# Optimization experiments

Measured on AMD Instinct MI355X. Metric: run time of the kernel, lower is better.

The kernel has to match this reference:

```python
import jax, jax.numpy as jnp
import numpy as np

D_MODEL = 1024
N_HEADS = 16
HEAD_DIM = D_MODEL // N_HEADS
SCALE = HEAD_DIM ** -0.5
NEG = -9e15


def setup_inputs() -> dict:
    key = jax.random.key(0)
    k1, k2, k3 = jax.random.split(key, 3)
    B, S = 4, 2048
    x = jax.random.normal(k1, (B, S, D_MODEL), dtype=jnp.float32)
    W_qkv = jax.random.normal(k2, (D_MODEL, 3 * D_MODEL), dtype=jnp.float32) * (D_MODEL ** -0.5)
    b_qkv = jnp.zeros((3 * D_MODEL,), dtype=jnp.float32)
    W_out = jax.random.normal(k3, (D_MODEL, D_MODEL), dtype=jnp.float32) * (D_MODEL ** -0.5)
    b_out = jnp.zeros((D_MODEL,), dtype=jnp.float32)
    return {"x": x, "W_qkv": W_qkv, "b_qkv": b_qkv, "W_out": W_out, "b_out": b_out}


def reference(x, W_qkv, b_qkv, W_out, b_out):
    B, S, _ = x.shape
    qkv = x @ W_qkv + b_qkv                      # [B,S,3D]
    q, k, v = jnp.split(qkv, 3, axis=-1)
    def heads(t):
        return t.reshape(B, S, N_HEADS, HEAD_DIM).transpose(0, 2, 1, 3)  # [B,H,S,d]
    q, k, v = heads(q), heads(k), heads(v)
    logits = jnp.einsum('bhqd,bhkd->bhqk', q, k) * SCALE
    causal = jnp.tril(jnp.ones((S, S), dtype=bool))
    logits = jnp.where(causal[None, None], logits, jnp.float32(NEG))
    attn = jax.nn.softmax(logits, axis=-1)       # dropout p=0 -> identity
    vals = jnp.einsum('bhqk,bhkd->bhqd', attn, v)
    vals = vals.transpose(0, 2, 1, 3).reshape(B, S, D_MODEL)
    return vals @ W_out + b_out
```

## Files before the change

kernel.cpp:

```cpp
#include <hip/hip_runtime.h>

typedef unsigned short u16;
typedef unsigned int u32;
typedef __attribute__((ext_vector_type(8))) short bf16x8;
typedef __attribute__((ext_vector_type(4))) float f32x4;

#define MFMA16(a, b, c) __builtin_amdgcn_mfma_f32_16x16x32_bf16((a), (b), (c), 0, 0, 0)

constexpr int D = 1024;
constexpr int NH = 16;
constexpr int HD = 64;
constexpr int BB = 4;
constexpr int SS = 2048;
constexpr int BH = BB * NH;
constexpr int MTOK = BB * SS;
constexpr float SCALE_LOG2E = 0.125f * 1.44269504088896340736f;

__device__ __forceinline__ u16 f32_bf16(float f) {
  union { float f; u32 u; } v; v.f = f;
  u32 u = v.u;
  u += 0x7FFFu + ((u >> 16) & 1u);
  return (u16)(u >> 16);
}

__device__ __forceinline__ float exp2_fast(float x) {
  float r; asm("v_exp_f32 %0, %1" : "=v"(r) : "v"(x)); return r;
}
__device__ __forceinline__ u16 cvt_bf16_1(float f) {
  u32 r; asm("v_cvt_pk_bf16_f32 %0, %1, %1" : "=v"(r) : "v"(f)); return (u16)r;
}

__device__ __forceinline__ void gload_lds16(const void* g, u16* l) {
  __builtin_amdgcn_global_load_lds(
      (const __attribute__((address_space(1))) u32*)g,
      (__attribute__((address_space(3))) u32*)l, 16, 0, 0);
}

__global__ __launch_bounds__(256)
void cvt_bf16(const float* __restrict__ in, u16* __restrict__ out, int n4) {
  int i = blockIdx.x * 256 + threadIdx.x;
  const int stride = gridDim.x * 256;
  for (; i < n4; i += stride) {
    float4 v = reinterpret_cast<const float4*>(in)[i];
    u32 lo = (u32)f32_bf16(v.x) | ((u32)f32_bf16(v.y) << 16);
    u32 hi = (u32)f32_bf16(v.z) | ((u32)f32_bf16(v.w) << 16);
    reinterpret_cast<uint2*>(out)[i] = make_uint2(lo, hi);
  }
}

__global__ __launch_bounds__(256)
void transpose_bf16(const float* __restrict__ in, u16* __restrict__ out, int R, int C) {
  __shared__ float tile[32][33];
  const int c0 = blockIdx.x * 32, r0 = blockIdx.y * 32;
  const int tx = threadIdx.x, ty = threadIdx.y;
#pragma unroll
  for (int i = 0; i < 4; i++)
    tile[ty + 8 * i][tx] = in[(size_t)(r0 + ty + 8 * i) * C + c0 + tx];
  __syncthreads();
#pragma unroll
  for (int i = 0; i < 4; i++)
    out[(size_t)(c0 + ty + 8 * i) * R + r0 + tx] = f32_bf16(tile[tx][ty + 8 * i]);
}

template <int MODE>
__global__ __launch_bounds__(256)
void gemm_bf16(const u16* __restrict__ A, const u16* __restrict__ Bt,
               const float* __restrict__ bias,
               u16* __restrict__ q_out, u16* __restrict__ k_out,
               u16* __restrict__ vt_out, float* __restrict__ f_out,
               int M, int N, int K) {
  constexpr int BK = 32;
  __shared__ u16 lds_a[3][128 * BK];
  __shared__ u16 lds_b[3][128 * BK];
  const int m0 = blockIdx.x * 128;
  const int n0 = blockIdx.y * 128;
  const int t = threadIdx.x;
  const int lane = t & 63;
  const int w = t >> 6;
  const int wr = w >> 1, wc = w & 1;
  const int fr = lane & 15, fq = lane >> 4;

  const int srow = t >> 2;
  const int schunk = (t & 3) ^ ((srow >> 1) & 3);
  const u16* ga0 = A + (size_t)(m0 + srow) * K + schunk * 8;
  const u16* ga1 = ga0 + (size_t)64 * K;
  const u16* gb0 = Bt + (size_t)(n0 + srow) * K + schunk * 8;
  const u16* gb1 = gb0 + (size_t)64 * K;

  const int swz = ((fr >> 1) & 3) << 4;

#define GSTAGE(bufi, koff)                                                    \
  {                                                                           \
    gload_lds16(ga0 + (koff), lds_a[bufi] + t * 8);                           \
    gload_lds16(ga1 + (koff), lds_a[bufi] + (t + 256) * 8);                   \
    gload_lds16(gb0 + (koff), lds_b[bufi] + t * 8);                           \
    gload_lds16(gb1 + (koff), lds_b[bufi] + (t + 256) * 8);                   \
  }

  f32x4 acc[4][4] = {};
  const int nt = K / BK;

  GSTAGE(0, 0);
  GSTAGE(1, BK);

  int cur = 0;
  for (int kt = 0; kt < nt; ++kt) {
    if (kt + 1 < nt)
      asm volatile("s_waitcnt vmcnt(4)" ::: "memory");
    else
      asm volatile("s_waitcnt vmcnt(0)" ::: "memory");
    __builtin_amdgcn_s_barrier();
    __builtin_amdgcn_sched_barrier(0);

    const char* ca = (const char*)lds_a[cur];
    const char* cb = (const char*)lds_b[cur];
    bf16x8 af[4], bfr[4];
#pragma unroll
    for (int i = 0; i < 4; i++)
      af[i] = *reinterpret_cast<const bf16x8*>(
          ca + (wr * 64 + i * 16 + fr) * 64 + ((fq * 16) ^ swz));
#pragma unroll
    for (int i = 0; i < 4; i++)
      bfr[i] = *reinterpret_cast<const bf16x8*>(
          cb + (wc * 64 + i * 16 + fr) * 64 + ((fq * 16) ^ swz));
    __builtin_amdgcn_s_setprio(1);
#pragma unroll
    for (int i = 0; i < 4; i++)
#pragma unroll
      for (int j = 0; j < 4; j++)
        acc[i][j] = MFMA16(af[i], bfr[j], acc[i][j]);
    __builtin_amdgcn_s_setprio(0);

    if (kt + 2 < nt) {
      const int bufn = cur >= 1 ? cur - 1 : 2;
      GSTAGE(bufn, (kt + 2) * BK);
    }
    cur = cur == 2 ? 0 : cur + 1;
  }
#undef GSTAGE

#pragma unroll
  for (int i = 0; i < 4; i++) {
#pragma unroll
    for (int j = 0; j < 4; j++) {
      const int ncol = n0 + wc * 64 + j * 16 + fr;
      const float bs = bias[ncol];
#pragma unroll
      for (int r = 0; r < 4; r++) {
        const int mrow = m0 + wr * 64 + i * 16 + fq * 4 + r;
        const float vv = acc[i][j][r] + bs;
        if (MODE == 0) {
          const int which = ncol >> 10;
          const int rem = ncol & 1023;
          const int hh = rem >> 6, dd = rem & 63;
          const int bb = mrow >> 11, ss = mrow & 2047;
          const int bh = bb * 16 + hh;
          if (which == 0)
            q_out[((size_t)bh * SS + ss) * HD + dd] = f32_bf16(vv * SCALE_LOG2E);
          else if (which == 1)
            k_out[((size_t)bh * SS + ss) * HD + dd] = f32_bf16(vv);
          else
            vt_out[((size_t)bh * HD + dd) * SS + ss] = f32_bf16(vv);
        } else {
          f_out[(size_t)mrow * N + ncol] = vv;
        }
      }
    }
  }
}

__global__ __launch_bounds__(512)
void attn_fwd(const u16* __restrict__ Qb, const u16* __restrict__ Kb,
              const u16* __restrict__ Vt, u16* __restrict__ vals) {
  const int bid = blockIdx.x;
  const int wk = (bid & 7) * 64 + (bid >> 3);
  const int bh = wk >> 3;
  const int pA = wk & 7;
  const int qtA = pA, qtB = 15 - pA;
  const int nA = 2 * qtA + 2;
  const int nTot = 34;
  const u16* Qp = Qb + (size_t)bh * SS * HD;
  const char* Kp = (const char*)(Kb + (size_t)bh * SS * HD);
  const char* Vp = (const char*)(Vt + (size_t)bh * HD * SS);
  const int t = threadIdx.x, lane = t & 63, w = t >> 6;
  const int fr = lane & 15, fq = lane >> 4;
  const int swz = (fr & 7) << 4;

  __shared__ u16 kbuf[3][4096];
  __shared__ u16 vbuf[3][4096];
  __shared__ u16 plds[8][16][72];
  u16* myp = &plds[w][0][0];

  const int lin = t * 16;

  int offKV[8];
#pragma unroll
  for (int kf = 0; kf < 4; kf++)
#pragma unroll
    for (int kk = 0; kk < 2; kk++)
      offKV[kf * 2 + kk] = (kf * 16 + fr) * 128 + ((kk * 64 + fq * 16) ^ swz);

  bf16x8 aq[2];
  {
    const int qbase = qtA * 128 + w * 16;
#pragma unroll
    for (int kk = 0; kk < 2; kk++)
      aq[kk] = *reinterpret_cast<const bf16x8*>(Qp + (size_t)(qbase + fr) * HD + kk * 32 + fq * 8);
  }

  f32x4 o[4] = {};
  float mrun[4], lpart[4];
#pragma unroll
  for (int j = 0; j < 4; j++) { mrun[j] = -3e38f; lpart[j] = 0.f; }

#define STAGE(bufi, kvt_)                                                     \
  {                                                                           \
    const int row = lin >> 7, colb = lin & 127;                               \
    const int scol = colb ^ ((row & 7) << 4);                                 \
    gload_lds16(Kp + (size_t)((kvt_) * 64 + row) * 128 + scol,                \
                &kbuf[bufi][lin >> 1]);                                       \
    gload_lds16(Vp + (size_t)row * 4096 + (kvt_) * 128 + scol,                \
                &vbuf[bufi][lin >> 1]);                                       \
  }
#define KVIDX(ti_) ((ti_) >= nA ? (ti_) - nA : (ti_))

  auto write_out = [&](int qt) {
    const int b_ = bh >> 4, h_ = bh & 15;
    const int qb = qt * 128 + w * 16;
    float linv[4];
#pragma unroll
    for (int j = 0; j < 4; j++) {
      float rs = lpart[j];
#pragma unroll
      for (int off = 1; off < 16; off <<= 1)
        rs += __shfl_xor(rs, off, 64);
      linv[j] = 1.f / rs;
    }
#pragma unroll
    for (int df = 0; df < 4; df++)
#pragma unroll
      for (int j = 0; j < 4; j++) {
        const float vv = o[df][j] * linv[j];
        const int qg = qb + fq * 4 + j;
        vals[((size_t)(b_ * SS + qg)) * D + h_ * HD + df * 16 + fr] = cvt_bf16_1(vv);
      }
  };

  int cur = 0;
  STAGE(0, 0);
  STAGE(1, 1);

  for (int ti = 0; ti < nTot; ++ti) {
    const bool segB = ti >= nA;
    const int kvt = segB ? ti - nA : ti;
    const int qt = segB ? qtB : qtA;

    if (ti + 1 < nTot)
      asm volatile("s_waitcnt vmcnt(2)" ::: "memory");
    else
      asm volatile("s_waitcnt vmcnt(0)" ::: "memory");
    __builtin_amdgcn_s_barrier();
    __builtin_amdgcn_sched_barrier(0);

    if (ti == nA) {
      write_out(qtA);
      const int qbase = qtB * 128 + w * 16;
#pragma unroll
      for (int kk = 0; kk < 2; kk++)
        aq[kk] = *reinterpret_cast<const bf16x8*>(Qp + (size_t)(qbase + fr) * HD + kk * 32 + fq * 8);
#pragma unroll
      for (int j = 0; j < 4; j++) { mrun[j] = -3e38f; lpart[j] = 0.f; }
#pragma unroll
      for (int df = 0; df < 4; df++) o[df] = f32x4{0.f, 0.f, 0.f, 0.f};
    }

    const char* kb = (const char*)kbuf[cur];
    const char* vb = (const char*)vbuf[cur];

    f32x4 sc[4] = {};
    __builtin_amdgcn_s_setprio(1);
#pragma unroll
    for (int kf = 0; kf < 4; kf++) {
#pragma unroll
      for (int kk = 0; kk < 2; kk++) {
        bf16x8 bk = *reinterpret_cast<const bf16x8*>(kb + offKV[kf * 2 + kk]);
        sc[kf] = MFMA16(aq[kk], bk, sc[kf]);
      }
    }
    __builtin_amdgcn_s_setprio(0);
    if ((kvt >> 1) == qt) {
      const int kg0 = kvt * 64 + fr;
      const int rg0 = qt * 128 + w * 16 + fq * 4;
#pragma unroll
      for (int kf = 0; kf < 4; kf++)
#pragma unroll
        for (int j = 0; j < 4; j++)
          if (kg0 + kf * 16 > rg0 + j) sc[kf][j] = -3e38f;
    }
    float mj[4];
#pragma unroll
    for (int j = 0; j < 4; j++) {
      float m = fmaxf(fmaxf(sc[0][j], sc[1][j]), fmaxf(sc[2][j], sc[3][j]));
#pragma unroll
      for (int off = 1; off < 16; off <<= 1)
        m = fmaxf(m, __shfl_xor(m, off, 64));
      mj[j] = m;
    }
    const bool need = (mj[0] > mrun[0] + 8.f) | (mj[1] > mrun[1] + 8.f) |
                      (mj[2] > mrun[2] + 8.f) | (mj[3] > mrun[3] + 8.f);
    if (__any((int)need)) {
#pragma unroll
      for (int j = 0; j < 4; j++) {
        const float mnew = fmaxf(mrun[j], mj[j]);
        const float alpha = exp2_fast(mrun[j] - mnew);
        mrun[j] = mnew;
        lpart[j] *= alpha;
#pragma unroll
        for (int df = 0; df < 4; df++) o[df][j] *= alpha;
      }
    }
#pragma unroll
    for (int j = 0; j < 4; j++) {
#pragma unroll
      for (int kf = 0; kf < 4; kf++) {
        const float p = exp2_fast(sc[kf][j] - mrun[j]);
        sc[kf][j] = p;
        lpart[j] += p;
      }
    }
#pragma unroll
    for (int kf = 0; kf < 4; kf++)
#pragma unroll
      for (int j = 0; j < 4; j++)
        myp[(fq * 4 + j) * 72 + kf * 16 + fr] = cvt_bf16_1(sc[kf][j]);
    bf16x8 pa[2];
#pragma unroll
    for (int kk = 0; kk < 2; kk++)
      pa[kk] = *reinterpret_cast<const bf16x8*>(myp + fr * 72 + kk * 32 + fq * 8);
    __builtin_amdgcn_s_setprio(1);
#pragma unroll
    for (int df = 0; df < 4; df++) {
#pragma unroll
      for (int kk = 0; kk < 2; kk++) {
        bf16x8 bv = *reinterpret_cast<const bf16x8*>(vb + offKV[df * 2 + kk]);
        o[df] = MFMA16(pa[kk], bv, o[df]);
      }
    }
    __builtin_amdgcn_s_setprio(0);

    const int nxt = ti + 2;
    if (nxt < nTot) {
      const int bufn = cur >= 1 ? cur - 1 : 2;
      STAGE(bufn, KVIDX(nxt));
    }
    cur = cur == 2 ? 0 : cur + 1;
  }
  write_out(qtB);
#undef STAGE
#undef KVIDX
}

extern "C" void kernel_launch(void* const* d_in, const int* in_sizes, int n_in,
                              void* d_out, int out_size, void* d_ws, size_t ws_size,
                              hipStream_t stream) {
  const float* x = (const float*)d_in[0];
  const float* Wqkv = (const float*)d_in[1];
  const float* bqkv = (const float*)d_in[2];
  const float* Wout = (const float*)d_in[3];
  const float* bout = (const float*)d_in[4];
  float* out = (float*)d_out;

  char* p = (char*)d_ws;
  u16* xb = (u16*)p;    p += (size_t)MTOK * D * 2;
  u16* wqkvT = (u16*)p; p += (size_t)3 * D * D * 2;
  u16* woutT = (u16*)p; p += (size_t)D * D * 2;
  u16* Qb = (u16*)p;    p += (size_t)BH * SS * HD * 2;
  u16* Kb = (u16*)p;    p += (size_t)BH * SS * HD * 2;
  u16* Vt = (u16*)p;    p += (size_t)BH * SS * HD * 2;
  u16* vals = (u16*)p;  p += (size_t)MTOK * D * 2;

  cvt_bf16<<<2048, 256, 0, stream>>>(x, xb, MTOK * D / 4);
  transpose_bf16<<<dim3(3 * D / 32, D / 32), dim3(32, 8), 0, stream>>>(Wqkv, wqkvT, D, 3 * D);
  transpose_bf16<<<dim3(D / 32, D / 32), dim3(32, 8), 0, stream>>>(Wout, woutT, D, D);
  gemm_bf16<0><<<dim3(MTOK / 128, 3 * D / 128), 256, 0, stream>>>(
      xb, wqkvT, bqkv, Qb, Kb, Vt, nullptr, MTOK, 3 * D, D);
  attn_fwd<<<dim3(512), 512, 0, stream>>>(Qb, Kb, Vt, vals);
  gemm_bf16<1><<<dim3(MTOK / 128, D / 128), 256, 0, stream>>>(
      vals, woutT, bout, nullptr, nullptr, nullptr, out, MTOK, D, D);
}
```

Baseline: 192.1 us.

## Transpose QK^T MFMA so each lane owns one query row in softmax

Swaps the MFMA operand order for the score computation so the accumulator layout gives each lane a single query row across key columns. The row max and row sum then need only two cross-lane shuffles instead of four per row, per-row state shrinks to scalars, and P is written to LDS as packed bf16 pairs. Rescale factors and the final normalizer are broadcast back to the O layout with shuffles, which adds some shuffle work when rescaling and at output time.

```diff
diff --git a/kernel.cpp b/kernel.cpp
--- a/kernel.cpp
+++ b/kernel.cpp
@@ -28,6 +28,9 @@
 }
 __device__ __forceinline__ u16 cvt_bf16_1(float f) {
   u32 r; asm("v_cvt_pk_bf16_f32 %0, %1, %1" : "=v"(r) : "v"(f)); return (u16)r;
+}
+__device__ __forceinline__ u32 cvt_pk2(float lo, float hi) {
+  u32 r; asm("v_cvt_pk_bf16_f32 %0, %1, %2" : "=v"(r) : "v"(lo), "v"(hi)); return r;
 }
 
 __device__ __forceinline__ void gload_lds16(const void* g, u16* l) {
@@ -209,9 +212,7 @@
   }
 
   f32x4 o[4] = {};
-  float mrun[4], lpart[4];
-#pragma unroll
-  for (int j = 0; j < 4; j++) { mrun[j] = -3e38f; lpart[j] = 0.f; }
+  float mrun = -3e38f, lpart = 0.f;
 
 #define STAGE(bufi, kvt_)                                                     \
   {                                                                           \
@@ -227,20 +228,19 @@
   auto write_out = [&](int qt) {
     const int b_ = bh >> 4, h_ = bh & 15;
     const int qb = qt * 128 + w * 16;
-    float linv[4];
-#pragma unroll
-    for (int j = 0; j < 4; j++) {
-      float rs = lpart[j];
-#pragma unroll
-      for (int off = 1; off < 16; off <<= 1)
-        rs += __shfl_xor(rs, off, 64);
-      linv[j] = 1.f / rs;
-    }
+    float rs = lpart;
+    rs += __shfl_xor(rs, 16, 64);
+    rs += __shfl_xor(rs, 32, 64);
+    const float linv = 1.f / rs;
+    float lj[4];
+#pragma unroll
+    for (int j = 0; j < 4; j++)
+      lj[j] = __shfl(linv, (lane & 48) + fq * 4 + j, 64);
 #pragma unroll
     for (int df = 0; df < 4; df++)
 #pragma unroll
       for (int j = 0; j < 4; j++) {
-        const float vv = o[df][j] * linv[j];
+        const float vv = o[df][j] * lj[j];
         const int qg = qb + fq * 4 + j;
         vals[((size_t)(b_ * SS + qg)) * D + h_ * HD + df * 16 + fr] = cvt_bf16_1(vv);
       }
@@ -268,8 +268,7 @@
 #pragma unroll
       for (int kk = 0; kk < 2; kk++)
         aq[kk] = *reinterpret_cast<const bf16x8*>(Qp + (size_t)(qbase + fr) * HD + kk * 32 + fq * 8);
-#pragma unroll
-      for (int j = 0; j < 4; j++) { mrun[j] = -3e38f; lpart[j] = 0.f; }
+      mrun = -3e38f; lpart = 0.f;
 #pragma unroll
       for (int df = 0; df < 4; df++) o[df] = f32x4{0.f, 0.f, 0.f, 0.f};
     }
@@ -284,55 +283,57 @@
 #pragma unroll
       for (int kk = 0; kk < 2; kk++) {
         bf16x8 bk = *reinterpret_cast<const bf16x8*>(kb + offKV[kf * 2 + kk]);
-        sc[kf] = MFMA16(aq[kk], bk, sc[kf]);
+        sc[kf] = MFMA16(bk, aq[kk], sc[kf]);
       }
     }
     __builtin_amdgcn_s_setprio(0);
     if ((kvt >> 1) == qt) {
-      const int kg0 = kvt * 64 + fr;
-      const int rg0 = qt * 128 + w * 16 + fq * 4;
+      const int qg = qt * 128 + w * 16 + fr;
+      const int kg0 = kvt * 64 + fq * 4;
 #pragma unroll
       for (int kf = 0; kf < 4; kf++)
 #pragma unroll
         for (int j = 0; j < 4; j++)
-          if (kg0 + kf * 16 > rg0 + j) sc[kf][j] = -3e38f;
-    }
-    float mj[4];
-#pragma unroll
-    for (int j = 0; j < 4; j++) {
-      float m = fmaxf(fmaxf(sc[0][j], sc[1][j]), fmaxf(sc[2][j], sc[3][j]));
-#pragma unroll
-      for (int off = 1; off < 16; off <<= 1)
-        m = fmaxf(m, __shfl_xor(m, off, 64));
-      mj[j] = m;
-    }
-    const bool need = (mj[0] > mrun[0] + 8.f) | (mj[1] > mrun[1] + 8.f) |
-                      (mj[2] > mrun[2] + 8.f) | (mj[3] > mrun[3] + 8.f);
-    if (__any((int)need)) {
+          if (kg0 + kf * 16 + j > qg) sc[kf][j] = -3e38f;
+    }
+    float m = fmaxf(fmaxf(sc[0][0], sc[0][1]), fmaxf(sc[0][2], sc[0][3]));
+#pragma unroll
+    for (int kf = 1; kf < 4; kf++)
+      m = fmaxf(m, fmaxf(fmaxf(sc[kf][0], sc[kf][1]), fmaxf(sc[kf][2], sc[kf][3])));
+    m = fmaxf(m, __shfl_xor(m, 16, 64));
+    m = fmaxf(m, __shfl_xor(m, 32, 64));
+    if (__any((int)(m > mrun + 8.f))) {
+      const float mnew = fmaxf(mrun, m);
+      const float alpha = exp2_fast(mrun - mnew);
+      mrun = mnew;
+      lpart *= alpha;
+      float aj[4];
+#pragma unroll
+      for (int j = 0; j < 4; j++)
+        aj[j] = __shfl(alpha, (lane & 48) + fq * 4 + j, 64);
+#pragma unroll
+      for (int df = 0; df < 4; df++)
+#pragma unroll
+        for (int j = 0; j < 4; j++) o[df][j] *= aj[j];
+    }
+#pragma unroll
+    for (int kf = 0; kf < 4; kf++)
 #pragma unroll
       for (int j = 0; j < 4; j++) {
-        const float mnew = fmaxf(mrun[j], mj[j]);
-        const float alpha = exp2_fast(mrun[j] - mnew);
-        mrun[j] = mnew;
-        lpart[j] *= alpha;
-#pragma unroll
-        for (int df = 0; df < 4; df++) o[df][j] *= alpha;
-      }
-    }
-#pragma unroll
-    for (int j = 0; j < 4; j++) {
+        const float p = exp2_fast(sc[kf][j] - mrun);
+        sc[kf][j] = p;
+        lpart += p;
+      }
+    {
+      u16* mypr = myp + fr * 72;
 #pragma unroll
       for (int kf = 0; kf < 4; kf++) {
-        const float p = exp2_fast(sc[kf][j] - mrun[j]);
-        sc[kf][j] = p;
-        lpart[j] += p;
-      }
-    }
-#pragma unroll
-    for (int kf = 0; kf < 4; kf++)
-#pragma unroll
-      for (int j = 0; j < 4; j++)
-        myp[(fq * 4 + j) * 72 + kf * 16 + fr] = cvt_bf16_1(sc[kf][j]);
+        const u32 p01 = cvt_pk2(sc[kf][0], sc[kf][1]);
+        const u32 p23 = cvt_pk2(sc[kf][2], sc[kf][3]);
+        *reinterpret_cast<u32*>(mypr + kf * 16 + fq * 4) = p01;
+        *reinterpret_cast<u32*>(mypr + kf * 16 + fq * 4 + 2) = p23;
+      }
+    }
     bf16x8 pa[2];
 #pragma unroll
     for (int kk = 0; kk < 2; kk++)
```

Result: faster. 171.8 us (median of 4 runs) (-10.6%).
